# Optimization experiments

Hardware: AMD Instinct MI355X
Metric: run time of the kernel (lower is better)

The kernel has to match this reference:

```python
import jax, jax.numpy as jnp
import numpy as np

B, S, D = 2, 4096, 2048
HEADS, HEAD_DIM = 16, 128
EPS = 1e-5


def setup_inputs() -> dict:
    key = jax.random.key(0)
    ks = jax.random.split(key, 8)
    hidden_states = jax.random.normal(ks[0], (B, S, D), dtype=jnp.float32)
    # rotary angles, broadcastable to [B, S, heads, head_dim]
    freqs_cis = jax.random.uniform(ks[1], (1, S, 1, HEAD_DIM), dtype=jnp.float32) * 6.283185
    scale = 1.0 / np.sqrt(D)
    # weights stored [in, out] (transpose of torch Linear weight)
    wq = jax.random.normal(ks[2], (D, HEADS * HEAD_DIM), dtype=jnp.float32) * scale
    wk = jax.random.normal(ks[3], (D, HEADS * HEAD_DIM), dtype=jnp.float32) * scale
    wv = jax.random.normal(ks[4], (D, HEADS * HEAD_DIM), dtype=jnp.float32) * scale
    norm_q_w = jnp.ones((HEAD_DIM,), dtype=jnp.float32)
    norm_k_w = jnp.ones((HEAD_DIM,), dtype=jnp.float32)
    w_out = jax.random.normal(ks[5], (HEADS * HEAD_DIM, D), dtype=jnp.float32) * scale
    b_out = jnp.zeros((D,), dtype=jnp.float32)
    return {"hidden_states": hidden_states, "freqs_cis": freqs_cis,
            "wq": wq, "wk": wk, "wv": wv,
            "norm_q_w": norm_q_w, "norm_k_w": norm_k_w,
            "w_out": w_out, "b_out": b_out}


def _rms_norm(x, w):
    var = jnp.mean(jnp.square(x), axis=-1, keepdims=True)
    return x * jax.lax.rsqrt(var + EPS) * w


def _apply_rotary(x, freqs_cis):
    rot_dim = freqs_cis.shape[-1]
    xr, x_pass = x[..., :rot_dim], x[..., rot_dim:]
    cos_ = jnp.cos(freqs_cis).astype(x.dtype)
    sin_ = jnp.sin(freqs_cis).astype(x.dtype)
    x1, x2 = jnp.split(xr, 2, axis=-1)
    x_rot = jnp.concatenate((-x2, x1), axis=-1)
    return jnp.concatenate((xr * cos_ + x_rot * sin_, x_pass), axis=-1)


def reference(hidden_states, freqs_cis, wq, wk, wv, norm_q_w, norm_k_w, w_out, b_out):
    b, s, _ = hidden_states.shape
    # QKV projections -> [B, S, H, Dh]
    q = (hidden_states @ wq).reshape(b, s, HEADS, HEAD_DIM)
    k = (hidden_states @ wk).reshape(b, s, HEADS, HEAD_DIM)
    v = (hidden_states @ wv).reshape(b, s, HEADS, HEAD_DIM)
    q = _rms_norm(q, norm_q_w)
    k = _rms_norm(k, norm_k_w)
    q = _apply_rotary(q, freqs_cis)
    k = _apply_rotary(k, freqs_cis)
    # SDPA with BSND layout, scale = 1/sqrt(head_dim)
    attn = jax.nn.dot_product_attention(q, k, v)  # [B, S, H, Dh]
    out = attn.reshape(b, s, HEADS * HEAD_DIM) @ w_out + b_out
    return out
```

## Files before the change

### kernel.cpp

```cpp
#include <hip/hip_runtime.h>
#include <stdint.h>


#define S_LEN  4096
#define NHEAD  16
#define HDIM   128
#define DMODEL 2048
#define MROWS  8192

typedef unsigned short u16;
typedef unsigned int   u32;
typedef __attribute__((ext_vector_type(4)))  float  f32x4;
typedef __attribute__((ext_vector_type(16))) float  f32x16;
typedef __attribute__((ext_vector_type(4)))  u16    u16x4;
typedef __attribute__((ext_vector_type(8)))  u16    u16x8;
typedef __attribute__((ext_vector_type(4)))  u32    u32x4;
typedef __attribute__((ext_vector_type(8)))  __bf16 bf16x8;

__device__ __forceinline__ u16 f2bf(float x){
  unsigned u = __builtin_bit_cast(unsigned, x);
  u += 0x7FFFu + ((u >> 16) & 1u);
  return (u16)(u >> 16);
}
__device__ __forceinline__ float bf2f(u16 b){
  unsigned u = ((unsigned)b) << 16;
  return __builtin_bit_cast(float, u);
}
__device__ __forceinline__ u32 cvtpk(float lo, float hi_){
  u32 r;
  asm("v_cvt_pk_bf16_f32 %0, %1, %2" : "=v"(r) : "v"(lo), "v"(hi_));
  return r;
}
__device__ __forceinline__ void gload16(const void* g, void* l){
  __builtin_amdgcn_global_load_lds((__attribute__((address_space(1))) void*)g,
                                   (__attribute__((address_space(3))) void*)l,
                                   16, 0, 0);
}

__global__ void k_cast_hs(const float* __restrict__ in, u16* __restrict__ out){
  size_t i = (size_t)blockIdx.x * 256 + threadIdx.x;
  const f32x4* p = (const f32x4*)in;
  f32x4 a = p[i*2], b = p[i*2+1];
  u16x8 o;
  o[0]=f2bf(a[0]); o[1]=f2bf(a[1]); o[2]=f2bf(a[2]); o[3]=f2bf(a[3]);
  o[4]=f2bf(b[0]); o[5]=f2bf(b[1]); o[6]=f2bf(b[2]); o[7]=f2bf(b[3]);
  ((u16x8*)out)[i] = o;
}

__global__ void k_transpose_w(const float* __restrict__ in, u16* __restrict__ out){
  __shared__ float t[64][65];
  const int tid = threadIdx.x;
  const int k0 = blockIdx.x * 64, n0 = blockIdx.y * 64;
#pragma unroll
  for (int it = 0; it < 4; ++it){
    int slot = it*256 + tid;
    int r = slot >> 4, c = (slot & 15) * 4;
    f32x4 v = *(const f32x4*)&in[(size_t)(k0+r)*DMODEL + n0 + c];
    t[r][c] = v[0]; t[r][c+1] = v[1]; t[r][c+2] = v[2]; t[r][c+3] = v[3];
  }
  __syncthreads();
#pragma unroll
  for (int it = 0; it < 2; ++it){
    int slot = it*256 + tid;
    int r = slot >> 3, c = (slot & 7) * 8;
    u16x8 o;
#pragma unroll
    for (int j = 0; j < 8; ++j) o[j] = f2bf(t[c+j][r]);
    *(u16x8*)&out[(size_t)(n0+r)*DMODEL + k0 + c] = o;
  }
}

__global__ void k_tables(const float* __restrict__ fr, float* __restrict__ cn,
                         float* __restrict__ sn){
  int i = blockIdx.x*256 + threadIdx.x;
  float f = fr[i];
  cn[i] = cosf(f); sn[i] = sinf(f);
}

__device__ __forceinline__ void gemm_loop(const u16* __restrict__ A,
                                          const u16* __restrict__ Bt,
                                          int m0, int n0,
                                          u16* Asm, u16* Bsm,
                                          f32x4 (&acc)[4][4], int lane, int wid){
  const int wr = wid >> 1, wc = wid & 1;
#pragma unroll 1
  for (int kt = 0; kt < DMODEL/64; ++kt){
#pragma unroll
    for (int it = 0; it < 4; ++it){
      int slot = it*256 + wid*64 + lane;
      int row = slot >> 3, cs = slot & 7;
      int ci = cs ^ (row & 7);
      gload16(A  + (size_t)(m0+row)*DMODEL + kt*64 + ci*8, Asm + (size_t)(it*256 + wid*64)*8);
      gload16(Bt + (size_t)(n0+row)*DMODEL + kt*64 + ci*8, Bsm + (size_t)(it*256 + wid*64)*8);
    }
    __syncthreads();
#pragma unroll
    for (int ks = 0; ks < 2; ++ks){
      bf16x8 af[4], bfv[4];
#pragma unroll
      for (int mt = 0; mt < 4; ++mt){
        int row = wr*64 + mt*16 + (lane & 15);
        int cs = (ks*4 + (lane >> 4)) ^ (row & 7);
        af[mt] = *(const bf16x8*)(Asm + ((size_t)row*8 + cs)*8);
      }
#pragma unroll
      for (int nt = 0; nt < 4; ++nt){
        int row = wc*64 + nt*16 + (lane & 15);
        int cs = (ks*4 + (lane >> 4)) ^ (row & 7);
        bfv[nt] = *(const bf16x8*)(Bsm + ((size_t)row*8 + cs)*8);
      }
#pragma unroll
      for (int mt = 0; mt < 4; ++mt)
#pragma unroll
        for (int nt = 0; nt < 4; ++nt)
          acc[mt][nt] = __builtin_amdgcn_mfma_f32_16x16x32_bf16(af[mt], bfv[nt], acc[mt][nt], 0, 0, 0);
    }
    __syncthreads();
  }
}

__global__ __launch_bounds__(256, 2)
void k_gemm_qkv(const u16* __restrict__ A, const u16* __restrict__ Bt,
                u16* __restrict__ qkp, u16* __restrict__ vt){
  __shared__ u16 Asm[128*64];
  __shared__ u16 Bsm[128*64];
  const int lane = threadIdx.x & 63, wid = threadIdx.x >> 6;
  const int m0 = blockIdx.x * 128, n0 = blockIdx.y * 128;
  f32x4 acc[4][4] = {};
  gemm_loop(A, Bt, m0, n0, Asm, Bsm, acc, lane, wid);
  const int wr = wid >> 1, wc = wid & 1;
  if (n0 < 2*DMODEL){
#pragma unroll
    for (int mt = 0; mt < 4; ++mt)
#pragma unroll
      for (int nt = 0; nt < 4; ++nt){
        int col = n0 + wc*64 + nt*16 + (lane & 15);
#pragma unroll
        for (int r = 0; r < 4; ++r){
          int row = m0 + wr*64 + mt*16 + (lane >> 4)*4 + r;
          qkp[(size_t)row*4096 + col] = f2bf(acc[mt][nt][r]);
        }
      }
  } else {
    const int hh = (n0 - 2*DMODEL) >> 7;
    const int b  = m0 >> 12;
#pragma unroll
    for (int mt = 0; mt < 4; ++mt)
#pragma unroll
      for (int nt = 0; nt < 4; ++nt){
        u16x4 pk;
#pragma unroll
        for (int r = 0; r < 4; ++r) pk[r] = f2bf(acc[mt][nt][r]);
        int d  = wc*64 + nt*16 + (lane & 15);
        int s_ = (m0 & (S_LEN-1)) + wr*64 + mt*16 + (lane >> 4)*4;
        *(u16x4*)&vt[(((size_t)b*NHEAD + hh)*HDIM + d)*S_LEN + s_] = pk;
      }
  }
}

__global__ __launch_bounds__(256)
void k_qk_post(const u16* __restrict__ qkp, const float* __restrict__ cn,
               const float* __restrict__ sn, const float* __restrict__ wqn,
               const float* __restrict__ wkn, u16* __restrict__ Qo, u16* __restrict__ Ko){
  const int lane = threadIdx.x & 63, wid = threadIdx.x >> 6;
  const int gw = blockIdx.x*4 + wid;
  const int row = gw >> 4;
  const int h  = gw & 15;
  const int s_ = row & (S_LEN-1);
  const int b  = row >> 12;
  const float c1 = cn[s_*HDIM + lane],      c2 = cn[s_*HDIM + 64 + lane];
  const float t1 = sn[s_*HDIM + lane],      t2 = sn[s_*HDIM + 64 + lane];
  const size_t ob = (((size_t)b*NHEAD + h)*S_LEN + s_)*HDIM;
  {
    const u16* p = qkp + (size_t)row*4096 + h*HDIM;
    float x1 = bf2f(p[lane]), x2 = bf2f(p[lane+64]);
    float ss = x1*x1 + x2*x2;
#pragma unroll
    for (int m = 1; m < 64; m <<= 1) ss += __shfl_xor(ss, m);
    float rn = rsqrtf(ss*(1.0f/128.0f) + 1e-5f);
    x1 *= rn * wqn[lane]; x2 *= rn * wqn[lane+64];
    const float qs = 0.12751743f;
    Qo[ob + lane]      = f2bf((x1*c1 - x2*t1) * qs);
    Qo[ob + 64 + lane] = f2bf((x2*c2 + x1*t2) * qs);
  }
  {
    const u16* p = qkp + (size_t)row*4096 + 2048 + h*HDIM;
    float x1 = bf2f(p[lane]), x2 = bf2f(p[lane+64]);
    float ss = x1*x1 + x2*x2;
#pragma unroll
    for (int m = 1; m < 64; m <<= 1) ss += __shfl_xor(ss, m);
    float rn = rsqrtf(ss*(1.0f/128.0f) + 1e-5f);
    x1 *= rn * wkn[lane]; x2 *= rn * wkn[lane+64];
    Ko[ob + lane]      = f2bf(x1*c1 - x2*t1);
    Ko[ob + 64 + lane] = f2bf(x2*c2 + x1*t2);
  }
}

__device__ __forceinline__ void stage_kv(const u16* __restrict__ Kg,
                                         const u16* __restrict__ Vt,
                                         size_t base, int kb,
                                         u16* Ksm, u16* Vsm, int lane, int wid){
#pragma unroll
  for (int it = 0; it < 4; ++it){
    int slot = it*256 + wid*64 + lane;
    { int row = slot >> 4, cs = slot & 15, ci = cs ^ (row & 7);
      gload16(Kg + base + (size_t)(kb*64 + row)*HDIM + ci*8, Ksm + (size_t)(it*256 + wid*64)*8); }
    { int row = slot >> 3, cs = slot & 7,  ci = cs ^ (row & 7);
      gload16(Vt + base + (size_t)row*S_LEN + kb*64 + ci*8,  Vsm + (size_t)(it*256 + wid*64)*8); }
  }
}

__global__ __launch_bounds__(256, 2)
void k_attn(const u16* __restrict__ Q, const u16* __restrict__ Kg,
            const u16* __restrict__ Vt, u16* __restrict__ Og){
  __shared__ u16 Ksm[2][64*128];
  __shared__ u16 Vsm[2][128*64];
  const int lane = threadIdx.x & 63, wid = threadIdx.x >> 6;
  const int col = lane & 31, hi = lane >> 5;
  const int bh = blockIdx.y;
  const int b = bh >> 4, h = bh & 15;
  const size_t base = (size_t)bh * S_LEN * HDIM;
  const int q0 = blockIdx.x * 128;
  const int qw = q0 + wid*32;

  stage_kv(Kg, Vt, base, 0, Ksm[0], Vsm[0], lane, wid);

  bf16x8 qb[8];
  {
    const u16* qp = Q + base + (size_t)(qw + col)*HDIM + hi*8;
#pragma unroll
    for (int ks = 0; ks < 8; ++ks) qb[ks] = *(const bf16x8*)(qp + ks*16);
  }
  f32x16 acc[4] = {};
  float lsum = 0.f;
  int cur = 0;

#pragma unroll 1
  for (int kb = 0; kb < S_LEN/64; ++kb){
    if (kb + 1 < S_LEN/64){
      stage_kv(Kg, Vt, base, kb + 1, Ksm[cur ^ 1], Vsm[cur ^ 1], lane, wid);
      asm volatile("s_waitcnt vmcnt(8)" ::: "memory");
    } else {
      asm volatile("s_waitcnt vmcnt(0)" ::: "memory");
    }
    __builtin_amdgcn_s_barrier();
    asm volatile("" ::: "memory");
    const u16* Ks = Ksm[cur];
    const u16* Vs = Vsm[cur];

    f32x16 s0 = {}, s1 = {};
    __builtin_amdgcn_s_setprio(1);
#pragma unroll
    for (int ks = 0; ks < 8; ++ks){
      int slot = (ks*2 + hi);
      int r0 = col;
      bf16x8 kf0 = *(const bf16x8*)(Ks + (size_t)r0*128 + (size_t)(slot ^ (r0 & 7))*8);
      s0 = __builtin_amdgcn_mfma_f32_32x32x16_bf16(kf0, qb[ks], s0, 0, 0, 0);
      int r1 = col + 32;
      bf16x8 kf1 = *(const bf16x8*)(Ks + (size_t)r1*128 + (size_t)(slot ^ (r1 & 7))*8);
      s1 = __builtin_amdgcn_mfma_f32_32x32x16_bf16(kf1, qb[ks], s1, 0, 0, 0);
    }
    __builtin_amdgcn_s_setprio(0);

    float p0[16], p1[16];
#pragma unroll
    for (int r = 0; r < 16; ++r){
      p0[r] = __builtin_amdgcn_exp2f(s0[r]);
      p1[r] = __builtin_amdgcn_exp2f(s1[r]);
      lsum += p0[r] + p1[r];
    }
    u32 cw0[8], cw1[8];
#pragma unroll
    for (int j = 0; j < 8; ++j){
      cw0[j] = cvtpk(p0[2*j], p0[2*j+1]);
      cw1[j] = cvtpk(p1[2*j], p1[2*j+1]);
    }
    bf16x8 pa[4];
#pragma unroll
    for (int ks = 0; ks < 4; ++ks){
      const u32* cw = (ks < 2) ? cw0 : cw1;
      const int c4 = (ks & 1) * 4;
      u32 n0 = hi ? cw[c4+2] : cw[c4+0];
      u32 n1 = hi ? cw[c4+3] : cw[c4+1];
      u32 s0w = hi ? cw[c4+0] : cw[c4+2];
      u32 s1w = hi ? cw[c4+1] : cw[c4+3];
      u32 f0 = __shfl_xor((int)s0w, 32);
      u32 f1 = __shfl_xor((int)s1w, 32);
      u32x4 w;
      w[0] = hi ? f0 : n0;
      w[1] = hi ? f1 : n1;
      w[2] = hi ? n0 : f0;
      w[3] = hi ? n1 : f1;
      pa[ks] = __builtin_bit_cast(bf16x8, w);
    }

    __builtin_amdgcn_s_setprio(1);
#pragma unroll
    for (int dt = 0; dt < 4; ++dt){
      int row = dt*32 + col;
      const u16* vb = Vs + (size_t)row*64;
      int sw = row & 7;
#pragma unroll
      for (int ks = 0; ks < 4; ++ks){
        bf16x8 vf = *(const bf16x8*)(vb + (size_t)((ks*2 + hi) ^ sw)*8);
        acc[dt] = __builtin_amdgcn_mfma_f32_32x32x16_bf16(pa[ks], vf, acc[dt], 0, 0, 0);
      }
    }
    __builtin_amdgcn_s_setprio(0);
    __builtin_amdgcn_s_barrier();
    asm volatile("" ::: "memory");
    cur ^= 1;
  }

  float tot = lsum + __shfl_xor(lsum, 32);
  float inv[16];
#pragma unroll
  for (int r = 0; r < 16; ++r){
    int qr = (r & 3) + 4*hi + 8*(r >> 2);
    inv[r] = 1.0f / __shfl(tot, qr);
  }
  const size_t orow0 = (size_t)b*S_LEN + q0 + wid*32;
#pragma unroll
  for (int dt = 0; dt < 4; ++dt){
    int d = h*HDIM + dt*32 + col;
#pragma unroll
    for (int r = 0; r < 16; ++r){
      int qr = (r & 3) + 4*hi + 8*(r >> 2);
      Og[(orow0 + qr)*DMODEL + d] = f2bf(acc[dt][r] * inv[r]);
    }
  }
}

__global__ __launch_bounds__(256, 2)
void k_gemm_out(const u16* __restrict__ A, const u16* __restrict__ Bt,
                const float* __restrict__ bias, float* __restrict__ out){
  __shared__ u16 Asm[128*64];
  __shared__ u16 Bsm[128*64];
  const int lane = threadIdx.x & 63, wid = threadIdx.x >> 6;
  const int m0 = blockIdx.x * 128, n0 = blockIdx.y * 128;
  f32x4 acc[4][4] = {};
  gemm_loop(A, Bt, m0, n0, Asm, Bsm, acc, lane, wid);
  const int wr = wid >> 1, wc = wid & 1;
  float bv[4];
#pragma unroll
  for (int nt = 0; nt < 4; ++nt) bv[nt] = bias[n0 + wc*64 + nt*16 + (lane & 15)];
#pragma unroll
  for (int mt = 0; mt < 4; ++mt)
#pragma unroll
    for (int nt = 0; nt < 4; ++nt){
      int col = n0 + wc*64 + nt*16 + (lane & 15);
#pragma unroll
      for (int r = 0; r < 4; ++r){
        int row = m0 + wr*64 + mt*16 + (lane >> 4)*4 + r;
        out[(size_t)row*DMODEL + col] = acc[mt][nt][r] + bv[nt];
      }
    }
}

extern "C" void kernel_launch(void* const* d_in, const int* in_sizes, int n_in,
                              void* d_out, int out_size, void* d_ws, size_t ws_size,
                              hipStream_t stream){
  const float* hs    = (const float*)d_in[0];
  const float* freqs = (const float*)d_in[1];
  const float* wq    = (const float*)d_in[2];
  const float* wk    = (const float*)d_in[3];
  const float* wv    = (const float*)d_in[4];
  const float* nqw   = (const float*)d_in[5];
  const float* nkw   = (const float*)d_in[6];
  const float* wo    = (const float*)d_in[7];
  const float* bo    = (const float*)d_in[8];
  float* out = (float*)d_out;

  char* ws = (char*)d_ws;
  u16*   hs_bf = (u16*)(ws + 0);
  u16*   wqkvT = (u16*)(ws + 33554432);
  u16*   woutT = (u16*)(ws + 58720256);
  float* cosn  = (float*)(ws + 67108864);
  float* sinn  = (float*)(ws + 69206016);
  u16*   qkp   = (u16*)(ws + 71303168);
  u16*   vt    = (u16*)(ws + 138412032);
  u16*   kbuf  = (u16*)(ws + 171966464);
  if (ws_size < 205520896ULL) return;
  u16* qbuf = hs_bf;
  u16* attn = qkp;

  k_cast_hs    <<<8192, 256, 0, stream>>>(hs, hs_bf);
  k_transpose_w<<<dim3(32,32), 256, 0, stream>>>(wq, wqkvT);
  k_transpose_w<<<dim3(32,32), 256, 0, stream>>>(wk, wqkvT + (size_t)DMODEL*DMODEL);
  k_transpose_w<<<dim3(32,32), 256, 0, stream>>>(wv, wqkvT + (size_t)2*DMODEL*DMODEL);
  k_transpose_w<<<dim3(32,32), 256, 0, stream>>>(wo, woutT);
  k_tables     <<<2048, 256, 0, stream>>>(freqs, cosn, sinn);
  k_gemm_qkv   <<<dim3(64,48), 256, 0, stream>>>(hs_bf, wqkvT, qkp, vt);
  k_qk_post    <<<32768, 256, 0, stream>>>(qkp, cosn, sinn, nqw, nkw, qbuf, kbuf);
  k_attn       <<<dim3(32,32), 256, 0, stream>>>(qbuf, kbuf, vt, attn);
  k_gemm_out   <<<dim3(64,16), 256, 0, stream>>>(attn, woutT, bo, out);
}
```

Before: 648.2 us.

## Double-buffer LDS tiles in GEMM loop to overlap global loads with MFMA

```diff
diff --git a/kernel.cpp b/kernel.cpp
--- a/kernel.cpp
+++ b/kernel.cpp
@@ -77,23 +77,39 @@
   cn[i] = cosf(f); sn[i] = sinf(f);
 }
 
+__device__ __forceinline__ void stage_ab(const u16* __restrict__ A,
+                                         const u16* __restrict__ Bt,
+                                         int m0, int n0, int kt,
+                                         u16* Asm, u16* Bsm, int lane, int wid){
+#pragma unroll
+  for (int it = 0; it < 4; ++it){
+    int slot = it*256 + wid*64 + lane;
+    int row = slot >> 3, cs = slot & 7;
+    int ci = cs ^ (row & 7);
+    gload16(A  + (size_t)(m0+row)*DMODEL + kt*64 + ci*8, Asm + (size_t)(it*256 + wid*64)*8);
+    gload16(Bt + (size_t)(n0+row)*DMODEL + kt*64 + ci*8, Bsm + (size_t)(it*256 + wid*64)*8);
+  }
+}
+
 __device__ __forceinline__ void gemm_loop(const u16* __restrict__ A,
                                           const u16* __restrict__ Bt,
                                           int m0, int n0,
-                                          u16* Asm, u16* Bsm,
+                                          u16 (*Asm)[128*64], u16 (*Bsm)[128*64],
                                           f32x4 (&acc)[4][4], int lane, int wid){
   const int wr = wid >> 1, wc = wid & 1;
+  stage_ab(A, Bt, m0, n0, 0, Asm[0], Bsm[0], lane, wid);
 #pragma unroll 1
   for (int kt = 0; kt < DMODEL/64; ++kt){
-#pragma unroll
-    for (int it = 0; it < 4; ++it){
-      int slot = it*256 + wid*64 + lane;
-      int row = slot >> 3, cs = slot & 7;
-      int ci = cs ^ (row & 7);
-      gload16(A  + (size_t)(m0+row)*DMODEL + kt*64 + ci*8, Asm + (size_t)(it*256 + wid*64)*8);
-      gload16(Bt + (size_t)(n0+row)*DMODEL + kt*64 + ci*8, Bsm + (size_t)(it*256 + wid*64)*8);
-    }
-    __syncthreads();
+    if (kt + 1 < DMODEL/64){
+      stage_ab(A, Bt, m0, n0, kt + 1, Asm[(kt + 1) & 1], Bsm[(kt + 1) & 1], lane, wid);
+      asm volatile("s_waitcnt vmcnt(8)" ::: "memory");
+    } else {
+      asm volatile("s_waitcnt vmcnt(0)" ::: "memory");
+    }
+    __builtin_amdgcn_s_barrier();
+    asm volatile("" ::: "memory");
+    const u16* As = Asm[kt & 1];
+    const u16* Bs = Bsm[kt & 1];
 #pragma unroll
     for (int ks = 0; ks < 2; ++ks){
       bf16x8 af[4], bfv[4];
@@ -101,13 +117,13 @@
       for (int mt = 0; mt < 4; ++mt){
         int row = wr*64 + mt*16 + (lane & 15);
         int cs = (ks*4 + (lane >> 4)) ^ (row & 7);
-        af[mt] = *(const bf16x8*)(Asm + ((size_t)row*8 + cs)*8);
+        af[mt] = *(const bf16x8*)(As + ((size_t)row*8 + cs)*8);
       }
 #pragma unroll
       for (int nt = 0; nt < 4; ++nt){
         int row = wc*64 + nt*16 + (lane & 15);
         int cs = (ks*4 + (lane >> 4)) ^ (row & 7);
-        bfv[nt] = *(const bf16x8*)(Bsm + ((size_t)row*8 + cs)*8);
+        bfv[nt] = *(const bf16x8*)(Bs + ((size_t)row*8 + cs)*8);
       }
 #pragma unroll
       for (int mt = 0; mt < 4; ++mt)
@@ -115,15 +131,16 @@
         for (int nt = 0; nt < 4; ++nt)
           acc[mt][nt] = __builtin_amdgcn_mfma_f32_16x16x32_bf16(af[mt], bfv[nt], acc[mt][nt], 0, 0, 0);
     }
-    __syncthreads();
+    __builtin_amdgcn_s_barrier();
+    asm volatile("" ::: "memory");
   }
 }
 
 __global__ __launch_bounds__(256, 2)
 void k_gemm_qkv(const u16* __restrict__ A, const u16* __restrict__ Bt,
                 u16* __restrict__ qkp, u16* __restrict__ vt){
-  __shared__ u16 Asm[128*64];
-  __shared__ u16 Bsm[128*64];
+  __shared__ u16 Asm[2][128*64];
+  __shared__ u16 Bsm[2][128*64];
   const int lane = threadIdx.x & 63, wid = threadIdx.x >> 6;
   const int m0 = blockIdx.x * 128, n0 = blockIdx.y * 128;
   f32x4 acc[4][4] = {};
@@ -334,8 +351,8 @@
 __global__ __launch_bounds__(256, 2)
 void k_gemm_out(const u16* __restrict__ A, const u16* __restrict__ Bt,
                 const float* __restrict__ bias, float* __restrict__ out){
-  __shared__ u16 Asm[128*64];
-  __shared__ u16 Bsm[128*64];
+  __shared__ u16 Asm[2][128*64];
+  __shared__ u16 Bsm[2][128*64];
   const int lane = threadIdx.x & 63, wid = threadIdx.x >> 6;
   const int m0 = blockIdx.x * 128, n0 = blockIdx.y * 128;
   f32x4 acc[4][4] = {};
```

New measurement: 655.6 us. About the same (+1.1%).
